# Kernel tuning notes

Measured on AMD Instinct MI355X. Metric: run time of the kernel, lower is better.

The kernel has to match this reference:

```python
import jax, jax.numpy as jnp
import numpy as np

NUM_HEADS = 32
NUM_KV_HEADS = 8
NUM_GROUPS = NUM_HEADS // NUM_KV_HEADS  # 4
HEAD_DIM = 64
HIDDEN = 2048
ROPE_THETA = 10000.0


def rotate_half(x):
    half = x.shape[-1] // 2
    x1, x2 = x[..., :half], x[..., half:]
    return jnp.concatenate([-x2, x1], axis=-1)


def rope_cos_sin(seq_len, dtype):
    inv_freq = 1.0 / (ROPE_THETA ** (jnp.arange(0, HEAD_DIM, 2, dtype=jnp.float32) / HEAD_DIM))
    pos = jnp.arange(seq_len, dtype=jnp.float32)
    freqs = jnp.outer(pos, inv_freq)          # [S, HEAD_DIM/2]
    emb = jnp.concatenate([freqs, freqs], axis=-1)  # [S, HEAD_DIM]
    return jnp.cos(emb).astype(dtype), jnp.sin(emb).astype(dtype)


def setup_inputs() -> dict:
    key = jax.random.key(0)
    k0, k1, k2, k3, k4 = jax.random.split(key, 5)
    B, S = 2, 2048
    scale = 0.02
    return {
        "hidden_states": jax.random.normal(k0, (B, S, HIDDEN), dtype=jnp.float32),
        "Wq": jax.random.normal(k1, (NUM_HEADS * HEAD_DIM, HIDDEN), dtype=jnp.float32) * scale,
        "Wk": jax.random.normal(k2, (NUM_KV_HEADS * HEAD_DIM, HIDDEN), dtype=jnp.float32) * scale,
        "Wv": jax.random.normal(k3, (NUM_KV_HEADS * HEAD_DIM, HIDDEN), dtype=jnp.float32) * scale,
        "Wo": jax.random.normal(k4, (HIDDEN, NUM_HEADS * HEAD_DIM), dtype=jnp.float32) * scale,
    }


def reference(hidden_states, Wq, Wk, Wv, Wo):
    B, S, _ = hidden_states.shape
    # projections (nn.Linear: x @ W.T)
    q = (hidden_states @ Wq.T).reshape(B, S, NUM_HEADS, HEAD_DIM).transpose(0, 2, 1, 3)
    k = (hidden_states @ Wk.T).reshape(B, S, NUM_KV_HEADS, HEAD_DIM).transpose(0, 2, 1, 3)
    v = (hidden_states @ Wv.T).reshape(B, S, NUM_KV_HEADS, HEAD_DIM).transpose(0, 2, 1, 3)

    cos, sin = rope_cos_sin(S, q.dtype)  # [S, HEAD_DIM]
    cos = cos[None, None]                # [1,1,S,HEAD_DIM]
    sin = sin[None, None]
    q = q * cos + rotate_half(q) * sin
    k = k * cos + rotate_half(k) * sin

    # GQA: repeat kv heads to match query heads (repeat_interleave on head dim)
    k = jnp.repeat(k, NUM_GROUPS, axis=1)  # [B, NUM_HEADS, S, HEAD_DIM]
    v = jnp.repeat(v, NUM_GROUPS, axis=1)

    scale = 1.0 / jnp.sqrt(jnp.asarray(HEAD_DIM, dtype=q.dtype))
    scores = jnp.einsum('bhqd,bhkd->bhqk', q, k) * scale  # [B,H,S,S]
    causal = jnp.tril(jnp.ones((S, S), dtype=bool))
    scores = jnp.where(causal[None, None], scores, jnp.asarray(-jnp.inf, dtype=scores.dtype))
    attn = jax.nn.softmax(scores, axis=-1)
    out = jnp.einsum('bhqk,bhkd->bhqd', attn, v)           # [B,H,S,D]
    out = out.transpose(0, 2, 1, 3).reshape(B, S, NUM_HEADS * HEAD_DIM)
    return out @ Wo.T
```

## Files before the change

### kernel.cpp

```cpp
#include <hip/hip_runtime.h>

#define S_LEN 2048
#define BATCH 2
#define NH 32
#define NKV 8
#define HD 64
#define HID 2048
#define NTOK (BATCH * S_LEN)
#define NQKV 3072
#define SC_Q 0.18033688011112042f

typedef __attribute__((ext_vector_type(8))) __bf16 bf16x8;
typedef __attribute__((ext_vector_type(4))) float f32x4;

__device__ inline ushort f2b(float f) {
    union { float f; unsigned u; } x{f};
    unsigned r = (x.u + 0x7fff + ((x.u >> 16) & 1)) >> 16;
    return (ushort)r;
}
__device__ inline float ex2(float x) { return __builtin_amdgcn_exp2f(x); }

__global__ __launch_bounds__(256) void cvt_all(const float* __restrict__ hidden,
                                               const float* __restrict__ Wq,
                                               const float* __restrict__ Wk,
                                               const float* __restrict__ Wv,
                                               const float* __restrict__ Wo,
                                               ushort* __restrict__ hb,
                                               ushort* __restrict__ wqkv,
                                               ushort* __restrict__ wo) {
    int bid = blockIdx.x;
    const float* src;
    ushort* dst;
    int off;
    if (bid < 8192)        { src = hidden; dst = hb;                              off = bid; }
    else if (bid < 12288)  { src = Wq;     dst = wqkv;                            off = bid - 8192; }
    else if (bid < 13312)  { src = Wk;     dst = wqkv + (size_t)2048 * 2048;      off = bid - 12288; }
    else if (bid < 14336)  { src = Wv;     dst = wqkv + (size_t)2560 * 2048;      off = bid - 13312; }
    else                   { src = Wo;     dst = wo;                              off = bid - 14336; }
    size_t i = (size_t)off * 256 + threadIdx.x;
    float4 v = reinterpret_cast<const float4*>(src)[i];
    ushort4 o;
    o.x = f2b(v.x); o.y = f2b(v.y); o.z = f2b(v.z); o.w = f2b(v.w);
    reinterpret_cast<ushort4*>(dst)[i] = o;
}

__device__ inline void gl_lds16(const void* g, void* l) {
    __builtin_amdgcn_global_load_lds((const __attribute__((address_space(1))) void*)g,
                                     (__attribute__((address_space(3))) void*)l, 16, 0, 0);
}

template<int WF32, int ROPE>
__global__ __launch_bounds__(256) void gemm_bt(const ushort* __restrict__ A,
                                               const ushort* __restrict__ B,
                                               void* __restrict__ C,
                                               ushort* __restrict__ Kd,
                                               ushort* __restrict__ Vd,
                                               int M, int N, int K) {
    __shared__ __align__(16) ushort As[128 * 64];
    __shared__ __align__(16) ushort Bs[128 * 64];
    const int tid = threadIdx.x, lane = tid & 63, w = tid >> 6;
    const int wr = w >> 1, wc = w & 1, l15 = lane & 15, lg = lane >> 4;

    const int nbx = gridDim.x;
    int lid = blockIdx.y * nbx + blockIdx.x;
    const int cpx = (nbx * gridDim.y) >> 3;
    int swz = (lid & 7) * cpx + (lid >> 3);
    const int m0 = (swz / nbx) * 128, n0 = (swz % nbx) * 128;

    const int lsw = ((lane & 7) ^ (lane >> 3)) * 8;
    const ushort* Ag = A + (size_t)(m0 + w * 8 + (lane >> 3)) * K + lsw;
    const ushort* Bg = B + (size_t)(n0 + w * 8 + (lane >> 3)) * K + lsw;
    ushort* lA = As + w * 512;
    ushort* lB = Bs + w * 512;

    f32x4 acc[4][4] = {};

    for (int k0 = 0; k0 < K; k0 += 64) {
        __syncthreads();
#pragma unroll
        for (int j = 0; j < 4; j++) {
            gl_lds16(Ag + (size_t)(j * 32) * K + k0, lA + j * 2048);
            gl_lds16(Bg + (size_t)(j * 32) * K + k0, lB + j * 2048);
        }
        __syncthreads();

        const char* pa = (const char*)As + (wr * 64 + l15) * 128;
        const char* pb = (const char*)Bs + (wc * 64 + l15) * 128;
        const int sw = (l15 & 7) * 16;
        bf16x8 af[2][4], bff[2][4];
#pragma unroll
        for (int i = 0; i < 4; i++)
#pragma unroll
            for (int ks = 0; ks < 2; ks++) {
                const int po = (ks * 64 + lg * 16) ^ sw;
                af[ks][i]  = *(const bf16x8*)(pa + i * 2048 + po);
                bff[ks][i] = *(const bf16x8*)(pb + i * 2048 + po);
            }
#pragma unroll
        for (int ks = 0; ks < 2; ks++)
#pragma unroll
            for (int i = 0; i < 4; i++)
#pragma unroll
                for (int j = 0; j < 4; j++)
                    acc[i][j] = __builtin_amdgcn_mfma_f32_16x16x32_bf16(af[ks][i], bff[ks][j], acc[i][j], 0, 0, 0);
    }

    const int mr = m0 + wr * 64 + lg * 4, nc = n0 + wc * 64 + l15;

    if (!ROPE) {
#pragma unroll
        for (int i = 0; i < 4; i++)
#pragma unroll
            for (int j = 0; j < 4; j++)
#pragma unroll
                for (int r = 0; r < 4; r++) {
                    size_t row = mr + i * 16 + r, col = nc + j * 16;
                    if (WF32) ((float*)C)[row * N + col] = acc[i][j][r];
                    else      ((ushort*)C)[row * N + col] = f2b(acc[i][j][r]);
                }
        return;
    }

    const int hq = (n0 + wc * 64) >> 6;
    if (hq < 40) {
        const bool isQ = hq < 32;
        const float fd0 = ex2(-(float)l15 * 0.4152410118609203f);
        const float fd1 = fd0 * 0.01f;
#pragma unroll
        for (int i = 0; i < 4; i++)
#pragma unroll
            for (int r = 0; r < 4; r++) {
                float pos = (float)((mr + i * 16 + r) & (S_LEN - 1));
#pragma unroll
                for (int jj = 0; jj < 2; jj++) {
                    float ang = pos * (jj ? fd1 : fd0);
                    float sv, cv;
                    __sincosf(ang, &sv, &cv);
                    float x1 = acc[i][jj][r], x2 = acc[i][jj + 2][r];
                    float y0 = x1 * cv - x2 * sv;
                    float y1 = x2 * cv + x1 * sv;
                    if (isQ) { y0 *= SC_Q; y1 *= SC_Q; }
                    acc[i][jj][r] = y0;
                    acc[i][jj + 2][r] = y1;
                }
            }
    }
    ushort* dst;
    int dstride, colb;
    if (hq < 32)      { dst = (ushort*)C; dstride = 2048; colb = nc; }
    else if (hq < 40) { dst = Kd;         dstride = 512;  colb = nc - 2048; }
    else              { dst = Vd;         dstride = 512;  colb = nc - 2560; }
#pragma unroll
    for (int i = 0; i < 4; i++)
#pragma unroll
        for (int j = 0; j < 4; j++)
#pragma unroll
            for (int r = 0; r < 4; r++) {
                size_t row = mr + i * 16 + r;
                dst[row * dstride + colb + j * 16] = f2b(acc[i][j][r]);
            }
}

__global__ __launch_bounds__(256) void transpose_v(const ushort* __restrict__ V,
                                                   ushort* __restrict__ Vt) {
    __shared__ ushort tile[32][33];
    int bz = blockIdx.z, b = bz >> 3, kvh = bz & 7;
    int s0 = blockIdx.x * 32, d0 = blockIdx.y * 32;
    int tx = threadIdx.x & 31, ty = threadIdx.x >> 5;
#pragma unroll
    for (int i = 0; i < 4; i++)
        tile[ty + i * 8][tx] = V[(size_t)(b * S_LEN + s0 + ty + i * 8) * 512 + kvh * 64 + d0 + tx];
    __syncthreads();
#pragma unroll
    for (int i = 0; i < 4; i++)
        Vt[((size_t)((b * 8 + kvh) * 64 + d0 + ty + i * 8)) * S_LEN + s0 + tx] = tile[tx][ty + i * 8];
}

__global__ __launch_bounds__(256) void attn_k(const ushort* __restrict__ Q,
                                              const ushort* __restrict__ Kc,
                                              const ushort* __restrict__ Vt,
                                              ushort* __restrict__ O) {
    __shared__ __align__(16) ushort K_lds[2][4096];
    __shared__ __align__(16) ushort V_lds[2][4096];
    const int lane = threadIdx.x & 63, w = threadIdx.x >> 6;
    const int l15 = lane & 15, lg = lane >> 4;

    int lid = blockIdx.y * 16 + blockIdx.x;
    int swz = (lid & 7) * 128 + (lid >> 3);
    const int bxs = swz & 15;
    const int bh = swz >> 4;
    const int b = bh >> 5, h = bh & 31, kvh = h >> 2;

    const ushort* kSrc[2];
    const ushort* vSrc[2];
    int dstU[2];
#pragma unroll
    for (int j = 0; j < 2; j++) {
        int u = w * 2 + j;
        int row = u * 8 + (lane >> 3);
        int po = (lane & 7) * 16;
        int fr = ((row & 3) | (((row >> 3) & 1) << 2)) << 4;
        int dus = (po ^ fr) >> 1;
        kSrc[j] = Kc + (size_t)(b * S_LEN + row) * 512 + kvh * 64 + dus;
        vSrc[j] = Vt + ((size_t)((b * 8 + kvh) * 64 + row)) * S_LEN + dus;
        dstU[j] = u * 512;
    }

    int fr_k = ((l15 & 3) | (((l15 >> 2) & 1) << 2)) << 4;
    int kbase = 1024 * (l15 >> 2) + 128 * (l15 & 3) + ((lg * 16) ^ (fr_k & 48));
    int k6 = (fr_k >> 6) & 1;
    int kb0 = kbase + 64 * k6, kb1 = kbase + 64 * (1 - k6);
    int fr_v = ((l15 & 3) | (((l15 >> 3) & 1) << 2)) << 4;
    int vbase = 128 * l15 + ((lg * 16) ^ (fr_v & 48));
    int v6 = (fr_v >> 6) & 1;
    int vb0 = vbase + 64 * v6, vb1 = vbase + 64 * (1 - v6);

    bf16x8 onesf;
#pragma unroll
    for (int i = 0; i < 8; i++) onesf[i] = (__bf16)1.0f;

    for (int half = 0; half < 2; ++half) {
        const int bx = half ? (31 - bxs) : bxs;
        const int q0 = bx * 64 + w * 16;
        const int qrow = q0 + l15;
        const int ktend = bx;

        const ushort* qp = Q + (size_t)(b * S_LEN + qrow) * HID + h * 64 + lg * 8;
        bf16x8 qf0 = *(const bf16x8*)qp;
        bf16x8 qf1 = *(const bf16x8*)(qp + 32);

        f32x4 ao[4] = {};
        f32x4 lsum = {};

#pragma unroll
        for (int j = 0; j < 2; j++) {
            gl_lds16(kSrc[j], &K_lds[0][dstU[j]]);
            gl_lds16(vSrc[j], &V_lds[0][dstU[j]]);
        }
        __syncthreads();
        int cur = 0;

        for (int kt = 0; kt <= ktend; ++kt) {
            const int kn = kt << 6;
            if (kt < ktend) {
                const int kn2 = kn + 64;
#pragma unroll
                for (int j = 0; j < 2; j++) {
                    gl_lds16(kSrc[j] + (size_t)kn2 * 512, &K_lds[cur ^ 1][dstU[j]]);
                    gl_lds16(vSrc[j] + kn2, &V_lds[cur ^ 1][dstU[j]]);
                }
            }

            const char* Kt = (const char*)K_lds[cur];
            const char* Vl = (const char*)V_lds[cur];

            bf16x8 kf0[4], kf1[4];
#pragma unroll
            for (int kc = 0; kc < 4; kc++) {
                const int kcst = 4096 * (kc >> 1) + 512 * (kc & 1);
                kf0[kc] = *(const bf16x8*)(Kt + kb0 + kcst);
                kf1[kc] = *(const bf16x8*)(Kt + kb1 + kcst);
            }

            f32x4 s[4];
#pragma unroll
            for (int kc = 0; kc < 4; kc++) {
                f32x4 z = {};
                z = __builtin_amdgcn_mfma_f32_16x16x32_bf16(kf0[kc], qf0, z, 0, 0, 0);
                z = __builtin_amdgcn_mfma_f32_16x16x32_bf16(kf1[kc], qf1, z, 0, 0, 0);
                s[kc] = z;
            }

            if (kt == ktend) {
#pragma unroll
                for (int kc = 0; kc < 4; kc++)
#pragma unroll
                    for (int r = 0; r < 4; r++) {
                        int kv = kn + ((kc >> 1) << 5) + (lg << 3) + ((kc & 1) << 2) + r;
                        s[kc][r] = (kv <= qrow) ? s[kc][r] : -INFINITY;
                    }
            }

            bf16x8 pf0, pf1;
#pragma unroll
            for (int r = 0; r < 4; r++) {
                pf0[r]     = (__bf16)ex2(s[0][r]);
                pf0[4 + r] = (__bf16)ex2(s[1][r]);
                pf1[r]     = (__bf16)ex2(s[2][r]);
                pf1[4 + r] = (__bf16)ex2(s[3][r]);
            }

            lsum = __builtin_amdgcn_mfma_f32_16x16x32_bf16(pf0, onesf, lsum, 0, 0, 0);
            lsum = __builtin_amdgcn_mfma_f32_16x16x32_bf16(pf1, onesf, lsum, 0, 0, 0);

#pragma unroll
            for (int dt = 0; dt < 4; dt++) {
                bf16x8 vf0 = *(const bf16x8*)(Vl + vb0 + dt * 2048);
                bf16x8 vf1 = *(const bf16x8*)(Vl + vb1 + dt * 2048);
                ao[dt] = __builtin_amdgcn_mfma_f32_16x16x32_bf16(pf0, vf0, ao[dt], 0, 0, 0);
                ao[dt] = __builtin_amdgcn_mfma_f32_16x16x32_bf16(pf1, vf1, ao[dt], 0, 0, 0);
            }

            __syncthreads();
            cur ^= 1;
        }

        float invr[4];
#pragma unroll
        for (int r = 0; r < 4; r++) invr[r] = 1.0f / lsum[r];
        ushort* ob = O + (size_t)(b * S_LEN + q0 + lg * 4) * HID + h * 64 + l15;
#pragma unroll
        for (int dt = 0; dt < 4; dt++)
#pragma unroll
            for (int r = 0; r < 4; r++) {
                union { __bf16 h; ushort u; } cv{(__bf16)(ao[dt][r] * invr[r])};
                ob[(size_t)r * HID + dt * 16] = cv.u;
            }
    }
}

extern "C" void kernel_launch(void* const* d_in, const int* in_sizes, int n_in,
                              void* d_out, int out_size, void* d_ws, size_t ws_size,
                              hipStream_t stream) {
    const float* hidden = (const float*)d_in[0];
    const float* Wq = (const float*)d_in[1];
    const float* Wk = (const float*)d_in[2];
    const float* Wv = (const float*)d_in[3];
    const float* Wo = (const float*)d_in[4];

    char* ws = (char*)d_ws;
    size_t off = 0;
    auto alloc = [&](size_t bytes) -> void* {
        void* p = ws + off;
        off += (bytes + 255) & ~(size_t)255;
        return p;
    };
    ushort* hb   = (ushort*)alloc((size_t)NTOK * HID * 2);
    ushort* wqkv = (ushort*)alloc((size_t)NQKV * 2048 * 2);
    ushort* wo   = (ushort*)alloc((size_t)2048 * 2048 * 2);
    ushort* Qb   = (ushort*)alloc((size_t)NTOK * 2048 * 2);
    ushort* Kb   = (ushort*)alloc((size_t)NTOK * 512 * 2);
    ushort* Vb   = (ushort*)alloc((size_t)NTOK * 512 * 2);
    ushort* Vtb  = (ushort*)alloc((size_t)NTOK * 512 * 2);
    ushort* AO   = (ushort*)alloc((size_t)NTOK * 2048 * 2);

    cvt_all<<<18432, 256, 0, stream>>>(hidden, Wq, Wk, Wv, Wo, hb, wqkv, wo);

    gemm_bt<0, 1><<<dim3(24, 32), 256, 0, stream>>>(hb, wqkv, Qb, Kb, Vb, NTOK, NQKV, 2048);

    transpose_v<<<dim3(S_LEN / 32, 2, BATCH * NKV), 256, 0, stream>>>(Vb, Vtb);

    attn_k<<<dim3(16, BATCH * NH), 256, 0, stream>>>(Qb, Kb, Vtb, AO);

    gemm_bt<1, 0><<<dim3(16, 32), 256, 0, stream>>>(AO, wo, d_out, nullptr, nullptr, NTOK, 2048, 2048);
}
```

Measured before the change: 186.0 us.

## Process both paired causal query tiles in one KV sweep sharing K/V loads

Instead of running two sequential passes over the key/value tiles for the low and high query blocks, the attention kernel now sweeps K/V once up to the longer block's extent and computes both query tiles against each loaded tile, with the shorter one masked off by a predicate after its end. This removes the repeated global-to-LDS loads and barriers for the shared prefix of key tiles. In exchange, register pressure roughly doubles for accumulators and probabilities, which may lower occupancy or cause spills.

```diff
diff --git a/kernel.cpp b/kernel.cpp
--- a/kernel.cpp
+++ b/kernel.cpp
@@ -219,104 +219,141 @@
 #pragma unroll
     for (int i = 0; i < 8; i++) onesf[i] = (__bf16)1.0f;
 
-    for (int half = 0; half < 2; ++half) {
-        const int bx = half ? (31 - bxs) : bxs;
-        const int q0 = bx * 64 + w * 16;
-        const int qrow = q0 + l15;
-        const int ktend = bx;
-
-        const ushort* qp = Q + (size_t)(b * S_LEN + qrow) * HID + h * 64 + lg * 8;
-        bf16x8 qf0 = *(const bf16x8*)qp;
-        bf16x8 qf1 = *(const bf16x8*)(qp + 32);
-
-        f32x4 ao[4] = {};
-        f32x4 lsum = {};
-
-#pragma unroll
-        for (int j = 0; j < 2; j++) {
-            gl_lds16(kSrc[j], &K_lds[0][dstU[j]]);
-            gl_lds16(vSrc[j], &V_lds[0][dstU[j]]);
-        }
-        __syncthreads();
-        int cur = 0;
-
-        for (int kt = 0; kt <= ktend; ++kt) {
-            const int kn = kt << 6;
-            if (kt < ktend) {
-                const int kn2 = kn + 64;
-#pragma unroll
-                for (int j = 0; j < 2; j++) {
-                    gl_lds16(kSrc[j] + (size_t)kn2 * 512, &K_lds[cur ^ 1][dstU[j]]);
-                    gl_lds16(vSrc[j] + kn2, &V_lds[cur ^ 1][dstU[j]]);
-                }
-            }
-
-            const char* Kt = (const char*)K_lds[cur];
-            const char* Vl = (const char*)V_lds[cur];
-
-            bf16x8 kf0[4], kf1[4];
-#pragma unroll
-            for (int kc = 0; kc < 4; kc++) {
-                const int kcst = 4096 * (kc >> 1) + 512 * (kc & 1);
-                kf0[kc] = *(const bf16x8*)(Kt + kb0 + kcst);
-                kf1[kc] = *(const bf16x8*)(Kt + kb1 + kcst);
-            }
-
-            f32x4 s[4];
+    const int ktA = bxs, ktB = 31 - bxs;
+    const int q0A = bxs * 64 + w * 16, q0B = (31 - bxs) * 64 + w * 16;
+    const int qrowA = q0A + l15, qrowB = q0B + l15;
+
+    const ushort* qpA = Q + (size_t)(b * S_LEN + qrowA) * HID + h * 64 + lg * 8;
+    const ushort* qpB = Q + (size_t)(b * S_LEN + qrowB) * HID + h * 64 + lg * 8;
+    bf16x8 qfA0 = *(const bf16x8*)qpA, qfA1 = *(const bf16x8*)(qpA + 32);
+    bf16x8 qfB0 = *(const bf16x8*)qpB, qfB1 = *(const bf16x8*)(qpB + 32);
+
+    f32x4 aoA[4] = {}, aoB[4] = {};
+    f32x4 lsumA = {}, lsumB = {};
+
+#pragma unroll
+    for (int j = 0; j < 2; j++) {
+        gl_lds16(kSrc[j], &K_lds[0][dstU[j]]);
+        gl_lds16(vSrc[j], &V_lds[0][dstU[j]]);
+    }
+    __syncthreads();
+    int cur = 0;
+
+    for (int kt = 0; kt <= ktB; ++kt) {
+        const int kn = kt << 6;
+        if (kt < ktB) {
+            const int kn2 = kn + 64;
+#pragma unroll
+            for (int j = 0; j < 2; j++) {
+                gl_lds16(kSrc[j] + (size_t)kn2 * 512, &K_lds[cur ^ 1][dstU[j]]);
+                gl_lds16(vSrc[j] + kn2, &V_lds[cur ^ 1][dstU[j]]);
+            }
+        }
+
+        const char* Kt = (const char*)K_lds[cur];
+        const char* Vl = (const char*)V_lds[cur];
+        const bool aAct = (kt <= ktA);
+
+        bf16x8 kf0[4], kf1[4];
+#pragma unroll
+        for (int kc = 0; kc < 4; kc++) {
+            const int kcst = 4096 * (kc >> 1) + 512 * (kc & 1);
+            kf0[kc] = *(const bf16x8*)(Kt + kb0 + kcst);
+            kf1[kc] = *(const bf16x8*)(Kt + kb1 + kcst);
+        }
+
+        f32x4 sB[4], sA[4];
+#pragma unroll
+        for (int kc = 0; kc < 4; kc++) {
+            f32x4 z = {};
+            z = __builtin_amdgcn_mfma_f32_16x16x32_bf16(kf0[kc], qfB0, z, 0, 0, 0);
+            z = __builtin_amdgcn_mfma_f32_16x16x32_bf16(kf1[kc], qfB1, z, 0, 0, 0);
+            sB[kc] = z;
+        }
+        if (aAct) {
 #pragma unroll
             for (int kc = 0; kc < 4; kc++) {
                 f32x4 z = {};
-                z = __builtin_amdgcn_mfma_f32_16x16x32_bf16(kf0[kc], qf0, z, 0, 0, 0);
-                z = __builtin_amdgcn_mfma_f32_16x16x32_bf16(kf1[kc], qf1, z, 0, 0, 0);
-                s[kc] = z;
-            }
-
-            if (kt == ktend) {
-#pragma unroll
-                for (int kc = 0; kc < 4; kc++)
-#pragma unroll
-                    for (int r = 0; r < 4; r++) {
-                        int kv = kn + ((kc >> 1) << 5) + (lg << 3) + ((kc & 1) << 2) + r;
-                        s[kc][r] = (kv <= qrow) ? s[kc][r] : -INFINITY;
-                    }
-            }
-
-            bf16x8 pf0, pf1;
+                z = __builtin_amdgcn_mfma_f32_16x16x32_bf16(kf0[kc], qfA0, z, 0, 0, 0);
+                z = __builtin_amdgcn_mfma_f32_16x16x32_bf16(kf1[kc], qfA1, z, 0, 0, 0);
+                sA[kc] = z;
+            }
+        }
+
+        if (kt == ktB) {
+#pragma unroll
+            for (int kc = 0; kc < 4; kc++)
+#pragma unroll
+                for (int r = 0; r < 4; r++) {
+                    int kv = kn + ((kc >> 1) << 5) + (lg << 3) + ((kc & 1) << 2) + r;
+                    sB[kc][r] = (kv <= qrowB) ? sB[kc][r] : -INFINITY;
+                }
+        }
+        if (kt == ktA) {
+#pragma unroll
+            for (int kc = 0; kc < 4; kc++)
+#pragma unroll
+                for (int r = 0; r < 4; r++) {
+                    int kv = kn + ((kc >> 1) << 5) + (lg << 3) + ((kc & 1) << 2) + r;
+                    sA[kc][r] = (kv <= qrowA) ? sA[kc][r] : -INFINITY;
+                }
+        }
+
+        bf16x8 pB0, pB1, pA0, pA1;
+#pragma unroll
+        for (int r = 0; r < 4; r++) {
+            pB0[r]     = (__bf16)ex2(sB[0][r]);
+            pB0[4 + r] = (__bf16)ex2(sB[1][r]);
+            pB1[r]     = (__bf16)ex2(sB[2][r]);
+            pB1[4 + r] = (__bf16)ex2(sB[3][r]);
+        }
+        if (aAct) {
 #pragma unroll
             for (int r = 0; r < 4; r++) {
-                pf0[r]     = (__bf16)ex2(s[0][r]);
-                pf0[4 + r] = (__bf16)ex2(s[1][r]);
-                pf1[r]     = (__bf16)ex2(s[2][r]);
-                pf1[4 + r] = (__bf16)ex2(s[3][r]);
-            }
-
-            lsum = __builtin_amdgcn_mfma_f32_16x16x32_bf16(pf0, onesf, lsum, 0, 0, 0);
-            lsum = __builtin_amdgcn_mfma_f32_16x16x32_bf16(pf1, onesf, lsum, 0, 0, 0);
-
-#pragma unroll
-            for (int dt = 0; dt < 4; dt++) {
-                bf16x8 vf0 = *(const bf16x8*)(Vl + vb0 + dt * 2048);
-                bf16x8 vf1 = *(const bf16x8*)(Vl + vb1 + dt * 2048);
-                ao[dt] = __builtin_amdgcn_mfma_f32_16x16x32_bf16(pf0, vf0, ao[dt], 0, 0, 0);
-                ao[dt] = __builtin_amdgcn_mfma_f32_16x16x32_bf16(pf1, vf1, ao[dt], 0, 0, 0);
-            }
-
-            __syncthreads();
-            cur ^= 1;
-        }
-
-        float invr[4];
-#pragma unroll
-        for (int r = 0; r < 4; r++) invr[r] = 1.0f / lsum[r];
-        ushort* ob = O + (size_t)(b * S_LEN + q0 + lg * 4) * HID + h * 64 + l15;
-#pragma unroll
-        for (int dt = 0; dt < 4; dt++)
-#pragma unroll
-            for (int r = 0; r < 4; r++) {
-                union { __bf16 h; ushort u; } cv{(__bf16)(ao[dt][r] * invr[r])};
-                ob[(size_t)r * HID + dt * 16] = cv.u;
-            }
-    }
+                pA0[r]     = (__bf16)ex2(sA[0][r]);
+                pA0[4 + r] = (__bf16)ex2(sA[1][r]);
+                pA1[r]     = (__bf16)ex2(sA[2][r]);
+                pA1[4 + r] = (__bf16)ex2(sA[3][r]);
+            }
+        }
+
+        lsumB = __builtin_amdgcn_mfma_f32_16x16x32_bf16(pB0, onesf, lsumB, 0, 0, 0);
+        lsumB = __builtin_amdgcn_mfma_f32_16x16x32_bf16(pB1, onesf, lsumB, 0, 0, 0);
+        if (aAct) {
+            lsumA = __builtin_amdgcn_mfma_f32_16x16x32_bf16(pA0, onesf, lsumA, 0, 0, 0);
+            lsumA = __builtin_amdgcn_mfma_f32_16x16x32_bf16(pA1, onesf, lsumA, 0, 0, 0);
+        }
+
+#pragma unroll
+        for (int dt = 0; dt < 4; dt++) {
+            bf16x8 vf0 = *(const bf16x8*)(Vl + vb0 + dt * 2048);
+            bf16x8 vf1 = *(const bf16x8*)(Vl + vb1 + dt * 2048);
+            aoB[dt] = __builtin_amdgcn_mfma_f32_16x16x32_bf16(pB0, vf0, aoB[dt], 0, 0, 0);
+            aoB[dt] = __builtin_amdgcn_mfma_f32_16x16x32_bf16(pB1, vf1, aoB[dt], 0, 0, 0);
+            if (aAct) {
+                aoA[dt] = __builtin_amdgcn_mfma_f32_16x16x32_bf16(pA0, vf0, aoA[dt], 0, 0, 0);
+                aoA[dt] = __builtin_amdgcn_mfma_f32_16x16x32_bf16(pA1, vf1, aoA[dt], 0, 0, 0);
+            }
+        }
+
+        __syncthreads();
+        cur ^= 1;
+    }
+
+    float invA[4], invB[4];
+#pragma unroll
+    for (int r = 0; r < 4; r++) { invA[r] = 1.0f / lsumA[r]; invB[r] = 1.0f / lsumB[r]; }
+    ushort* obA = O + (size_t)(b * S_LEN + q0A + lg * 4) * HID + h * 64 + l15;
+    ushort* obB = O + (size_t)(b * S_LEN + q0B + lg * 4) * HID + h * 64 + l15;
+#pragma unroll
+    for (int dt = 0; dt < 4; dt++)
+#pragma unroll
+        for (int r = 0; r < 4; r++) {
+            union { __bf16 h; ushort u; } cA{(__bf16)(aoA[dt][r] * invA[r])};
+            union { __bf16 h; ushort u; } cB{(__bf16)(aoB[dt][r] * invB[r])};
+            obA[(size_t)r * HID + dt * 16] = cA.u;
+            obB[(size_t)r * HID + dt * 16] = cB.u;
+        }
 }
 
 extern "C" void kernel_launch(void* const* d_in, const int* in_sizes, int n_in,
```

Measured after the change: 185.4 us. About the same (-0.3%).
